# Kernel optimization log

Hardware: AMD Instinct MI355X
Metric: run time of the kernel (lower is better)

Reference implementation:

```python
import jax, jax.numpy as jnp
import numpy as np

HEADS, DK, DV, STRIDE = 8, 32, 32, 2
EPS = 1e-5

def dwconv(x, w, b, stride):
    # depthwise 3x3, padding 1; w: [C,1,3,3]
    y = jax.lax.conv_general_dilated(
        x, w, (stride, stride), ((1, 1), (1, 1)),
        dimension_numbers=("NCHW", "OIHW", "NCHW"),
        feature_group_count=x.shape[1])
    return y + b[None, :, None, None]

def setup_inputs() -> dict:
    key = jax.random.key(0)
    ks = jax.random.split(key, 16)
    B_, C, H, W = 8, 256, 56, 56
    hd = HEADS * DK
    s = lambda k, shp: (jax.random.normal(k, shp, jnp.float32) * 0.02)
    return {
        "x": jax.random.normal(ks[0], (B_, C, H, W), jnp.float32),
        "Wk_dw": s(ks[1], (C, 1, 3, 3)), "bk_dw": jnp.zeros((C,), jnp.float32),
        "Wv_dw": s(ks[2], (C, 1, 3, 3)), "bv_dw": jnp.zeros((C,), jnp.float32),
        "Wq": s(ks[3], (hd, C)), "bq": jnp.zeros((hd,), jnp.float32),
        "Wk": s(ks[4], (hd, C)), "bk": jnp.zeros((hd,), jnp.float32),
        "Wv": s(ks[5], (HEADS * DV, C)), "bv": jnp.zeros((HEADS * DV,), jnp.float32),
        "Wo": s(ks[6], (C, HEADS * DV)), "bo": jnp.zeros((C,), jnp.float32),
        "Bbias": s(ks[7], (1, HEADS, H * W, (H // STRIDE) * (W // STRIDE))),
    }

def reference(x, Wk_dw, bk_dw, Wv_dw, bv_dw, Wq, bq, Wk, bk, Wv, bv, Wo, bo, Bbias):
    b, c, h, w = x.shape
    xr = x.reshape(b, c, h * w).transpose(0, 2, 1)  # [b, hw, c]
    # F.layer_norm with normalized_shape=(b, hw, c): single mean/var over ALL elements
    mu = jnp.mean(xr)
    var = jnp.mean((xr - mu) ** 2)
    xn = (xr - mu) * jax.lax.rsqrt(var + EPS)
    q = (xn @ Wq.T + bq).reshape(b, h * w, HEADS, DK).transpose(0, 2, 1, 3)  # [b,H,hw,dk]
    ki = dwconv(x, Wk_dw, bk_dw, STRIDE)
    kh, kw = ki.shape[2], ki.shape[3]
    kf = ki.reshape(b, c, kh * kw).transpose(0, 2, 1)
    k = (kf @ Wk.T + bk).reshape(b, kh * kw, HEADS, DK).transpose(0, 2, 1, 3)
    vi = dwconv(x, Wv_dw, bv_dw, STRIDE)
    vf = vi.reshape(b, c, kh * kw).transpose(0, 2, 1)
    v = (vf @ Wv.T + bv).reshape(b, kh * kw, HEADS, DV).transpose(0, 2, 1, 3)
    attn = jnp.einsum("bhid,bhjd->bhij", q, k) * (DK ** -0.5) + Bbias
    attn = jax.nn.softmax(attn, axis=-1)
    res = jnp.einsum("bhij,bhjd->bhid", attn, v).transpose(0, 2, 1, 3)
    res = res.reshape(b, h * w, HEADS * DV)
    out = (res @ Wo.T + bo).reshape(b, c, h, w)  # faithful to original .view (no transpose)
    return out + x
```

## Files before the change

kernel.cpp:

```cpp
#include <hip/hip_runtime.h>

typedef unsigned short u16;
typedef unsigned int   u32;
typedef __attribute__((ext_vector_type(8))) short short8;
typedef __attribute__((ext_vector_type(4))) float f32x4;

#define MFMA16(a, b, c) __builtin_amdgcn_mfma_f32_16x16x32_bf16((a), (b), (c), 0, 0, 0)

static constexpr int B_ = 8;
static constexpr int HW = 3136;
static constexpr int KW = 784;
static constexpr int NELEM = B_ * 256 * HW;

static constexpr size_t OFF_CNT = 4096;
static constexpr size_t OFF_W   = 8192;
static constexpr int AOFF_WQ = 0, AOFF_WK = 65536, AOFF_WV = 131072, AOFF_WO = 196608;
static constexpr int AOFF_WKDW = 262144, AOFF_WVDW = 264448;
static constexpr int AOFF_BKDW = 266752, AOFF_BVDW = 267008, AOFF_BQ = 267264;
static constexpr int AOFF_BK = 267520, AOFF_BV = 267776, AOFF_BO = 268032;
static constexpr size_t OFF_XT  = 557056;
static constexpr size_t SZ_XT   = (size_t)B_ * HW * 256 * 2;
static constexpr size_t SZ_KJ   = (size_t)B_ * KW * 256 * 2;
static constexpr size_t OFF_KIT = OFF_XT + SZ_XT;
static constexpr size_t OFF_VIT = OFF_KIT + SZ_KJ;
static constexpr size_t OFF_KI  = OFF_VIT + SZ_KJ;
static constexpr size_t OFF_VI  = OFF_KI + SZ_KJ;
static constexpr size_t OFF_Q   = OFF_VI + SZ_KJ;
static constexpr size_t OFF_O   = OFF_XT;

__device__ __forceinline__ float bf2f(u16 u) { return __uint_as_float(((u32)u) << 16); }
__device__ __forceinline__ u16 f2bf(float f) {
  u32 u = __float_as_uint(f);
  u32 r = u + 0x7FFFu + ((u >> 16) & 1u);
  return (u16)(r >> 16);
}
__device__ __forceinline__ float bflo(u32 u) { return __uint_as_float(u << 16); }
__device__ __forceinline__ float bfhi(u32 u) { return __uint_as_float(u & 0xFFFF0000u); }
__device__ __forceinline__ u32 packbf(float a, float b) {
  u32 ua = __float_as_uint(a); ua = (ua + 0x7FFFu + ((ua >> 16) & 1u)) >> 16;
  u32 ub = __float_as_uint(b); ub = (ub + 0x7FFFu + ((ub >> 16) & 1u)) >> 16;
  return ua | (ub << 16);
}

__global__ __launch_bounds__(256) void detect_k(const u32* __restrict__ x, int* __restrict__ cnt) {
  int c = 0;
  for (int i = threadIdx.x; i < 4096; i += 256) {
    float v = __uint_as_float(x[i] << 16);
    if (fabsf(v) > 1e4f) c++;
  }
#pragma unroll
  for (int off = 32; off > 0; off >>= 1) c += __shfl_down(c, off);
  if ((threadIdx.x & 63) == 0) atomicAdd(cnt, c);
}

struct CvtArgs { const void* src[12]; int dstoff[12]; int n[12]; };
__global__ __launch_bounds__(256) void cvtw_k(CvtArgs a, u16* __restrict__ arena,
                                              const int* __restrict__ cnt) {
  int t = blockIdx.y;
  int n = a.n[t];
  u16* d = arena + a.dstoff[t];
  int f32m = (*cnt >= 64);
  if (f32m) {
    const float* s = (const float*)a.src[t];
    for (int i = blockIdx.x * 256 + threadIdx.x; i < n; i += gridDim.x * 256) d[i] = f2bf(s[i]);
  } else {
    const u16* s = (const u16*)a.src[t];
    for (int i = blockIdx.x * 256 + threadIdx.x; i < n; i += gridDim.x * 256) d[i] = s[i];
  }
}

__global__ __launch_bounds__(256) void reduce_k(const void* __restrict__ x, double* __restrict__ acc,
                                                const int* __restrict__ cnt) {
  int f32m = (*cnt >= 64);
  float s = 0.f, ss = 0.f;
  if (f32m) {
    const float4* xv = (const float4*)x;
    const int n4 = NELEM / 4;
    for (int i = blockIdx.x * 256 + threadIdx.x; i < n4; i += gridDim.x * 256) {
      float4 u = xv[i];
      s += u.x + u.y + u.z + u.w;
      ss += u.x * u.x + u.y * u.y + u.z * u.z + u.w * u.w;
    }
  } else {
    const uint4* xv = (const uint4*)x;
    const int n8 = NELEM / 8;
    for (int i = blockIdx.x * 256 + threadIdx.x; i < n8; i += gridDim.x * 256) {
      uint4 u = xv[i];
      u32 w[4] = {u.x, u.y, u.z, u.w};
#pragma unroll
      for (int q = 0; q < 4; q++) {
        float f0 = __uint_as_float(w[q] << 16);
        float f1 = __uint_as_float(w[q] & 0xFFFF0000u);
        s += f0 + f1;
        ss += f0 * f0 + f1 * f1;
      }
    }
  }
#pragma unroll
  for (int off = 32; off > 0; off >>= 1) {
    s += __shfl_down(s, off);
    ss += __shfl_down(ss, off);
  }
  __shared__ float as_[4], ass_[4];
  int wv = threadIdx.x >> 6;
  if ((threadIdx.x & 63) == 0) { as_[wv] = s; ass_[wv] = ss; }
  __syncthreads();
  if (threadIdx.x == 0) {
    atomicAdd(acc + 0, (double)(as_[0] + as_[1] + as_[2] + as_[3]));
    atomicAdd(acc + 1, (double)(ass_[0] + ass_[1] + ass_[2] + ass_[3]));
  }
}

__global__ __launch_bounds__(256) void prep_k(const u16* __restrict__ wq, const u16* __restrict__ bq,
                                              float* __restrict__ wsf) {
  const double* acc = (const double*)wsf;
  __shared__ float sh[2];
  if (threadIdx.x == 0) {
    double N = (double)NELEM;
    double mu = acc[0] / N;
    double var = acc[1] / N - mu * mu;
    float rstd = (float)(1.0 / sqrt(var + 1e-5));
    sh[0] = (float)mu; sh[1] = rstd;
    wsf[4] = (float)mu; wsf[5] = rstd;
    wsf[6] = rstd * 0.17677669529663687f;
  }
  __syncthreads();
  int o = threadIdx.x;
  float wsum = 0.f;
  for (int c = 0; c < 256; c++) wsum += bf2f(wq[o * 256 + c]);
  wsf[16 + o] = (bf2f(bq[o]) - sh[1] * sh[0] * wsum) * 0.17677669529663687f;
}

__global__ __launch_bounds__(256) void transpose_x_k(const void* __restrict__ src, u16* __restrict__ dst,
                                                     const int* __restrict__ cnt) {
  int f32m = (*cnt >= 64);
  __shared__ u16 t[32][33];
  int b = blockIdx.z;
  int r0 = blockIdx.y * 32, c0 = blockIdx.x * 32;
  int tid = threadIdx.x, col = tid & 31;
  size_t base = (size_t)b * 256 * HW;
  if (f32m) {
    const float* s = (const float*)src + base;
#pragma unroll
    for (int i = 0; i < 4; i++) {
      int row = (tid >> 5) + i * 8;
      t[row][col] = f2bf(s[(size_t)(r0 + row) * HW + c0 + col]);
    }
  } else {
    const u16* s = (const u16*)src + base;
#pragma unroll
    for (int i = 0; i < 4; i++) {
      int row = (tid >> 5) + i * 8;
      t[row][col] = s[(size_t)(r0 + row) * HW + c0 + col];
    }
  }
  __syncthreads();
  u16* d = dst + base;
#pragma unroll
  for (int i = 0; i < 4; i++) {
    int row = (tid >> 5) + i * 8;
    d[(size_t)(c0 + row) * 256 + r0 + col] = t[col][row];
  }
}

__global__ __launch_bounds__(256) void transpose_kv_k(const u16* __restrict__ s1, u16* __restrict__ d1,
                                                      const u16* __restrict__ s2, u16* __restrict__ d2) {
  __shared__ u16 t[32][33];
  int which = blockIdx.z >> 3;
  int b = blockIdx.z & 7;
  const u16* src = which ? s2 : s1;
  u16* dst = which ? d2 : d1;
  int r0 = blockIdx.y * 32, c0 = blockIdx.x * 32;
  const u16* s = src + (size_t)b * 256 * KW;
  u16* d = dst + (size_t)b * 256 * KW;
  int tid = threadIdx.x, col = tid & 31;
#pragma unroll
  for (int i = 0; i < 4; i++) {
    int row = (tid >> 5) + i * 8;
    if (c0 + col < KW) t[row][col] = s[(size_t)(r0 + row) * KW + c0 + col];
  }
  __syncthreads();
#pragma unroll
  for (int i = 0; i < 4; i++) {
    int row = (tid >> 5) + i * 8;
    if (c0 + row < KW) d[(size_t)(c0 + row) * 256 + r0 + col] = t[col][row];
  }
}

__global__ __launch_bounds__(256) void dwconv_k(const void* __restrict__ x,
                                                const u16* __restrict__ arena,
                                                u16* __restrict__ ki, u16* __restrict__ vi,
                                                const int* __restrict__ cnt) {
  int f32m = (*cnt >= 64);
  int b = blockIdx.x >> 8;
  int c = blockIdx.x & 255;
  float wkf[9], wvf[9];
#pragma unroll
  for (int t = 0; t < 9; t++) {
    wkf[t] = bf2f(arena[AOFF_WKDW + c * 9 + t]);
    wvf[t] = bf2f(arena[AOFF_WVDW + c * 9 + t]);
  }
  float kb = bf2f(arena[AOFF_BKDW + c]), vb = bf2f(arena[AOFF_BVDW + c]);
  size_t xbase = (size_t)(b * 256 + c) * HW;
  auto body = [&](auto LDX) {
    for (int j = threadIdx.x; j < KW; j += 256) {
      int oi = j / 28, oj = j % 28;
      float ka = kb, va = vb;
#pragma unroll
      for (int di = 0; di < 3; di++) {
        int ii = 2 * oi - 1 + di;
        if ((unsigned)ii >= 56u) continue;
#pragma unroll
        for (int dj = 0; dj < 3; dj++) {
          int ij = 2 * oj - 1 + dj;
          if ((unsigned)ij >= 56u) continue;
          float xv = LDX(ii * 56 + ij);
          ka += xv * wkf[di * 3 + dj];
          va += xv * wvf[di * 3 + dj];
        }
      }
      ki[(size_t)(b * 256 + c) * KW + j] = f2bf(ka);
      vi[(size_t)(b * 256 + c) * KW + j] = f2bf(va);
    }
  };
  if (f32m) {
    const float* xp = (const float*)x + xbase;
    body([&](int i) { return xp[i]; });
  } else {
    const u16* xp = (const u16*)x + xbase;
    body([&](int i) { return bf2f(xp[i]); });
  }
}

__global__ __launch_bounds__(256) void proj_q_k(const u16* __restrict__ xt, const u16* __restrict__ Wq,
                                                const float* __restrict__ wsf, u16* __restrict__ q) {
  int lane = threadIdx.x & 63, wave = threadIdx.x >> 6;
  int l15 = lane & 15, quad = lane >> 4;
  int b = blockIdx.x / 49, pb = blockIdx.x % 49;
  int p0 = pb * 64 + wave * 16;
  const u16* arow = xt + ((size_t)(b * HW) + p0 + l15) * 256 + quad * 8;
  short8 af[8];
#pragma unroll
  for (int ks = 0; ks < 8; ks++) af[ks] = *(const short8*)(arow + ks * 32);
  float alpha = wsf[6];
  const float* beta = wsf + 16;
  for (int ot = 0; ot < 16; ot++) {
    const u16* brow = Wq + (size_t)(ot * 16 + l15) * 256 + quad * 8;
    f32x4 acc = {0.f, 0.f, 0.f, 0.f};
#pragma unroll
    for (int ks = 0; ks < 8; ks++) acc = MFMA16(af[ks], *(const short8*)(brow + ks * 32), acc);
    int o = ot * 16 + l15;
    float bet = beta[o];
    size_t base = ((size_t)(b * HW) + p0 + quad * 4) * 256 + o;
#pragma unroll
    for (int r = 0; r < 4; r++) q[base + (size_t)r * 256] = f2bf(alpha * acc[r] + bet);
  }
}

__global__ __launch_bounds__(256) void proj_k_k(const u16* __restrict__ kit, const u16* __restrict__ Wk,
                                                const u16* __restrict__ bk, u16* __restrict__ kout) {
  int lane = threadIdx.x & 63, wave = threadIdx.x >> 6;
  int l15 = lane & 15, quad = lane >> 4;
  int b = blockIdx.x / 13, jb = blockIdx.x % 13;
  int p0 = jb * 64 + wave * 16;
  if (p0 >= KW) return;
  const u16* arow = kit + ((size_t)(b * KW) + p0 + l15) * 256 + quad * 8;
  short8 af[8];
#pragma unroll
  for (int ks = 0; ks < 8; ks++) af[ks] = *(const short8*)(arow + ks * 32);
  for (int ot = 0; ot < 16; ot++) {
    const u16* brow = Wk + (size_t)(ot * 16 + l15) * 256 + quad * 8;
    f32x4 acc = {0.f, 0.f, 0.f, 0.f};
#pragma unroll
    for (int ks = 0; ks < 8; ks++) acc = MFMA16(af[ks], *(const short8*)(brow + ks * 32), acc);
    int o = ot * 16 + l15;
    float bias = bf2f(bk[o]);
    size_t base = ((size_t)(b * KW) + p0 + quad * 4) * 256 + o;
#pragma unroll
    for (int r = 0; r < 4; r++) kout[base + (size_t)r * 256] = f2bf(acc[r] + bias);
  }
}

__global__ __launch_bounds__(256) void proj_v_k(const u16* __restrict__ Wv, const u16* __restrict__ vit,
                                                const u16* __restrict__ bv, u16* __restrict__ vT) {
  int lane = threadIdx.x & 63, wave = threadIdx.x >> 6;
  int l15 = lane & 15, quad = lane >> 4;
  int b = blockIdx.x >> 4;
  int ob = (blockIdx.x >> 2) & 3;
  int js = blockIdx.x & 3;
  int o0 = ob * 64 + wave * 16;
  const u16* arow = Wv + (size_t)(o0 + l15) * 256 + quad * 8;
  short8 af[8];
#pragma unroll
  for (int ks = 0; ks < 8; ks++) af[ks] = *(const short8*)(arow + ks * 32);
  int jt0 = js * 13;
  int jt1 = (jt0 + 13 < 49) ? jt0 + 13 : 49;
  for (int jt = jt0; jt < jt1; jt++) {
    const u16* brow = vit + ((size_t)(b * KW) + jt * 16 + l15) * 256 + quad * 8;
    f32x4 acc = {0.f, 0.f, 0.f, 0.f};
#pragma unroll
    for (int ks = 0; ks < 8; ks++) acc = MFMA16(af[ks], *(const short8*)(brow + ks * 32), acc);
#pragma unroll
    for (int r = 0; r < 4; r++) {
      int o = o0 + quad * 4 + r;
      vT[((size_t)(b * 256) + o) * KW + jt * 16 + l15] = f2bf(acc[r] + bf2f(bv[o]));
    }
  }
}

static constexpr int BSTRIDE = 788;
__global__ __launch_bounds__(256) void attn_k(const u16* __restrict__ q, const u16* __restrict__ k,
                                              const u16* __restrict__ vT, const void* __restrict__ Bb,
                                              u16* __restrict__ Ob, const int* __restrict__ cnt) {
  int f32m = (*cnt >= 64);
  int tid = threadIdx.x;
  int lane = tid & 63, wave = tid >> 6;
  int l15 = lane & 15, quad = lane >> 4;
  int bid = blockIdx.x;
  int pt = bid >> 4;
  int h = (bid >> 1) & 7;
  int half = bid & 1;
  int b = half * 4 + wave;
  int p0 = pt * 16;
  __shared__ __align__(16) u16 bls[16 * BSTRIDE];
  __shared__ __align__(16) u16 Pch[4][16][40];

  {
    size_t boff = ((size_t)(h * HW) + p0) * KW;
    if (f32m) {
      const float* bbf = (const float*)Bb + boff;
#pragma unroll
      for (int it = 0; it < 13; it++) {
        int chunk = it * 256 + tid;
        if (chunk < 3136) {
          int row = chunk / 196, c4 = chunk - row * 196;
          float4 v = *(const float4*)(bbf + (size_t)row * KW + c4 * 4);
          uint2 p;
          p.x = packbf(v.x, v.y);
          p.y = packbf(v.z, v.w);
          *(uint2*)&bls[row * BSTRIDE + c4 * 4] = p;
        }
      }
    } else {
      const u16* bbb = (const u16*)Bb + boff;
#pragma unroll
      for (int it = 0; it < 13; it++) {
        int chunk = it * 256 + tid;
        if (chunk < 3136) {
          int row = chunk / 196, c4 = chunk - row * 196;
          *(uint2*)&bls[row * BSTRIDE + c4 * 4] = *(const uint2*)(bbb + (size_t)row * KW + c4 * 4);
        }
      }
    }
  }
  __syncthreads();

  const u16* qp = q + ((size_t)(b * HW) + p0 + l15) * 256 + h * 32 + quad * 8;
  short8 af = *(const short8*)qp;
  const u16* kb = k + (size_t)b * KW * 256 + h * 32 + quad * 8;

  u32 sp[49][2];
#pragma unroll
  for (int jt = 0; jt < 49; jt++) {
    short8 bfr = *(const short8*)(kb + (size_t)(jt * 16 + l15) * 256);
    f32x4 acc = {0.f, 0.f, 0.f, 0.f};
    acc = MFMA16(af, bfr, acc);
    int col = jt * 16 + l15;
    float v0 = acc[0] + bf2f(bls[(quad * 4 + 0) * BSTRIDE + col]);
    float v1 = acc[1] + bf2f(bls[(quad * 4 + 1) * BSTRIDE + col]);
    float v2 = acc[2] + bf2f(bls[(quad * 4 + 2) * BSTRIDE + col]);
    float v3 = acc[3] + bf2f(bls[(quad * 4 + 3) * BSTRIDE + col]);
    sp[jt][0] = packbf(v0, v1);
    sp[jt][1] = packbf(v2, v3);
  }

  float m[4] = {-1e30f, -1e30f, -1e30f, -1e30f};
#pragma unroll
  for (int jt = 0; jt < 49; jt++) {
    m[0] = fmaxf(m[0], bflo(sp[jt][0])); m[1] = fmaxf(m[1], bfhi(sp[jt][0]));
    m[2] = fmaxf(m[2], bflo(sp[jt][1])); m[3] = fmaxf(m[3], bfhi(sp[jt][1]));
  }
#pragma unroll
  for (int off = 1; off < 16; off <<= 1)
#pragma unroll
    for (int r = 0; r < 4; r++) m[r] = fmaxf(m[r], __shfl_xor(m[r], off));
  float l[4] = {0.f, 0.f, 0.f, 0.f};
#pragma unroll
  for (int jt = 0; jt < 49; jt++) {
    float e0 = __expf(bflo(sp[jt][0]) - m[0]);
    float e1 = __expf(bfhi(sp[jt][0]) - m[1]);
    float e2 = __expf(bflo(sp[jt][1]) - m[2]);
    float e3 = __expf(bfhi(sp[jt][1]) - m[3]);
    l[0] += e0; l[1] += e1; l[2] += e2; l[3] += e3;
    sp[jt][0] = packbf(e0, e1);
    sp[jt][1] = packbf(e2, e3);
  }
#pragma unroll
  for (int off = 1; off < 16; off <<= 1)
#pragma unroll
    for (int r = 0; r < 4; r++) l[r] += __shfl_xor(l[r], off);
  float inv[4];
#pragma unroll
  for (int r = 0; r < 4; r++) inv[r] = 1.f / l[r];

  f32x4 oa = {0.f, 0.f, 0.f, 0.f}, obb = {0.f, 0.f, 0.f, 0.f};
  const u16* vb = vT + ((size_t)(b * 256) + h * 32) * KW;
#pragma unroll
  for (int ch = 0; ch < 25; ch++) {
#pragma unroll
    for (int hf = 0; hf < 2; hf++) {
      int jt = ch * 2 + hf;
      u32 p0k = 0, p1k = 0;
      if (jt < 49) { p0k = sp[jt][0]; p1k = sp[jt][1]; }
      int col = hf * 16 + l15;
      Pch[wave][quad * 4 + 0][col] = (u16)(p0k & 0xFFFFu);
      Pch[wave][quad * 4 + 1][col] = (u16)(p0k >> 16);
      Pch[wave][quad * 4 + 2][col] = (u16)(p1k & 0xFFFFu);
      Pch[wave][quad * 4 + 3][col] = (u16)(p1k >> 16);
    }
    __syncthreads();
    short8 pf = *(const short8*)(&Pch[wave][l15][quad * 8]);
    int jo = ch * 32 + quad * 8;
    if (jo > 776) jo = 776;
    short8 v0 = *(const short8*)(vb + (size_t)l15 * KW + jo);
    short8 v1 = *(const short8*)(vb + (size_t)(16 + l15) * KW + jo);
    oa  = MFMA16(pf, v0, oa);
    obb = MFMA16(pf, v1, obb);
    __syncthreads();
  }
  size_t obase = ((size_t)(b * HW) + p0 + quad * 4) * 256 + h * 32 + l15;
#pragma unroll
  for (int r = 0; r < 4; r++) {
    Ob[obase + (size_t)r * 256]      = f2bf(oa[r] * inv[r]);
    Ob[obase + (size_t)r * 256 + 16] = f2bf(obb[r] * inv[r]);
  }
}

__global__ __launch_bounds__(256) void proj_o_k(const u16* __restrict__ Ob, const u16* __restrict__ Wo,
                                                const u16* __restrict__ bo, const void* __restrict__ x,
                                                void* __restrict__ out, const int* __restrict__ cnt) {
  int f32m = (*cnt >= 64);
  int lane = threadIdx.x & 63, wave = threadIdx.x >> 6;
  int l15 = lane & 15, quad = lane >> 4;
  int b = blockIdx.x / 49, pb = blockIdx.x % 49;
  int p0 = pb * 64 + wave * 16;
  const u16* arow = Ob + ((size_t)(b * HW) + p0 + l15) * 256 + quad * 8;
  short8 af[8];
#pragma unroll
  for (int ks = 0; ks < 8; ks++) af[ks] = *(const short8*)(arow + ks * 32);
  for (int ot = 0; ot < 16; ot++) {
    const u16* brow = Wo + (size_t)(ot * 16 + l15) * 256 + quad * 8;
    f32x4 acc = {0.f, 0.f, 0.f, 0.f};
#pragma unroll
    for (int ks = 0; ks < 8; ks++) acc = MFMA16(af[ks], *(const short8*)(brow + ks * 32), acc);
    int o = ot * 16 + l15;
    float bias = bf2f(bo[o]);
    if (f32m) {
      const float* xf = (const float*)x;
      float* of = (float*)out;
#pragma unroll
      for (int r = 0; r < 4; r++) {
        size_t idx = ((size_t)(b * HW) + p0 + quad * 4 + r) * 256 + o;
        of[idx] = acc[r] + bias + xf[idx];
      }
    } else {
      const u16* xb = (const u16*)x;
      u16* ob_ = (u16*)out;
#pragma unroll
      for (int r = 0; r < 4; r++) {
        size_t idx = ((size_t)(b * HW) + p0 + quad * 4 + r) * 256 + o;
        ob_[idx] = f2bf(acc[r] + bias + bf2f(xb[idx]));
      }
    }
  }
}

extern "C" void kernel_launch(void* const* d_in, const int* in_sizes, int n_in,
                              void* d_out, int out_size, void* d_ws, size_t ws_size,
                              hipStream_t stream) {
  (void)in_sizes; (void)n_in; (void)out_size; (void)ws_size;
  const void* x = d_in[0];
  char* ws = (char*)d_ws;
  int* cnt = (int*)(ws + OFF_CNT);
  u16* arena = (u16*)(ws + OFF_W);
  u16* xt  = (u16*)(ws + OFF_XT);
  u16* kit = (u16*)(ws + OFF_KIT);
  u16* vit = (u16*)(ws + OFF_VIT);
  u16* ki  = (u16*)(ws + OFF_KI);
  u16* vi  = (u16*)(ws + OFF_VI);
  u16* qb  = (u16*)(ws + OFF_Q);
  u16* Obuf = (u16*)(ws + OFF_O);

  CvtArgs a;
  const int srcidx[12] = {5, 7, 9, 11, 1, 3, 2, 4, 6, 8, 10, 12};
  const int dofs[12] = {AOFF_WQ, AOFF_WK, AOFF_WV, AOFF_WO, AOFF_WKDW, AOFF_WVDW,
                        AOFF_BKDW, AOFF_BVDW, AOFF_BQ, AOFF_BK, AOFF_BV, AOFF_BO};
  const int ns[12] = {65536, 65536, 65536, 65536, 2304, 2304, 256, 256, 256, 256, 256, 256};
  for (int i = 0; i < 12; i++) { a.src[i] = d_in[srcidx[i]]; a.dstoff[i] = dofs[i]; a.n[i] = ns[i]; }

  hipMemsetAsync(d_ws, 0, 8192, stream);
  detect_k<<<1, 256, 0, stream>>>((const u32*)x, cnt);
  cvtw_k<<<dim3(32, 12), 256, 0, stream>>>(a, arena, cnt);
  reduce_k<<<1024, 256, 0, stream>>>(x, (double*)d_ws, cnt);
  prep_k<<<1, 256, 0, stream>>>(arena + AOFF_WQ, arena + AOFF_BQ, (float*)d_ws);
  transpose_x_k<<<dim3(98, 8, 8), 256, 0, stream>>>(x, xt, cnt);
  dwconv_k<<<2048, 256, 0, stream>>>(x, arena, ki, vi, cnt);
  transpose_kv_k<<<dim3(25, 8, 16), 256, 0, stream>>>(ki, kit, vi, vit);
  proj_k_k<<<104, 256, 0, stream>>>(kit, arena + AOFF_WK, arena + AOFF_BK, ki);
  proj_v_k<<<128, 256, 0, stream>>>(arena + AOFF_WV, vit, arena + AOFF_BV, vi);
  proj_q_k<<<392, 256, 0, stream>>>(xt, arena + AOFF_WQ, (const float*)d_ws, qb);
  attn_k<<<3136, 256, 0, stream>>>(qb, ki, vi, d_in[13], Obuf, cnt);
  proj_o_k<<<392, 256, 0, stream>>>(Obuf, arena + AOFF_WO, arena + AOFF_BO, x, d_out, cnt);
}
```

Baseline: 534.8 us.

## Stage projection weights in LDS and stream attention softmax in chunks

Folds the Q, K and output projections into one templated kernel. Each block loads a 64-row slice of the weight matrix into shared memory once and reuses it across many row tiles, where before every wave reread weights from global memory. The attention kernel now uses an online softmax over 7 chunks of 128 keys and stores the bias tile transposed in LDS. This replaces the 49-tile register array and the per-chunk __syncthreads with a wave-local waitcnt, to lower register pressure and raise occupancy. It risks fewer blocks for the projections, and LDS bank conflicts on the transposed bias writes.

Result: no change. 531.7 us (-0.6%).

```diff
diff --git a/kernel.cpp b/kernel.cpp
--- a/kernel.cpp
+++ b/kernel.cpp
@@ -232,52 +232,75 @@
   }
 }
 
-__global__ __launch_bounds__(256) void proj_q_k(const u16* __restrict__ xt, const u16* __restrict__ Wq,
-                                                const float* __restrict__ wsf, u16* __restrict__ q) {
-  int lane = threadIdx.x & 63, wave = threadIdx.x >> 6;
+template<int MODE>
+__global__ __launch_bounds__(256, 4) void proj2_k(const u16* __restrict__ act, const u16* __restrict__ Wt,
+                                                  const float* __restrict__ wsf, const u16* __restrict__ bias,
+                                                  const void* __restrict__ x, void* __restrict__ outp,
+                                                  const int* __restrict__ cnt, int R, int tpb) {
+  __shared__ __align__(16) u16 Wl[64 * 264];
+  int tid = threadIdx.x, lane = tid & 63, wave = tid >> 6;
   int l15 = lane & 15, quad = lane >> 4;
-  int b = blockIdx.x / 49, pb = blockIdx.x % 49;
-  int p0 = pb * 64 + wave * 16;
-  const u16* arow = xt + ((size_t)(b * HW) + p0 + l15) * 256 + quad * 8;
-  short8 af[8];
-#pragma unroll
-  for (int ks = 0; ks < 8; ks++) af[ks] = *(const short8*)(arow + ks * 32);
-  float alpha = wsf[6];
-  const float* beta = wsf + 16;
-  for (int ot = 0; ot < 16; ot++) {
-    const u16* brow = Wq + (size_t)(ot * 16 + l15) * 256 + quad * 8;
-    f32x4 acc = {0.f, 0.f, 0.f, 0.f};
-#pragma unroll
-    for (int ks = 0; ks < 8; ks++) acc = MFMA16(af[ks], *(const short8*)(brow + ks * 32), acc);
-    int o = ot * 16 + l15;
-    float bet = beta[o];
-    size_t base = ((size_t)(b * HW) + p0 + quad * 4) * 256 + o;
-#pragma unroll
-    for (int r = 0; r < 4; r++) q[base + (size_t)r * 256] = f2bf(alpha * acc[r] + bet);
-  }
-}
-
-__global__ __launch_bounds__(256) void proj_k_k(const u16* __restrict__ kit, const u16* __restrict__ Wk,
-                                                const u16* __restrict__ bk, u16* __restrict__ kout) {
-  int lane = threadIdx.x & 63, wave = threadIdx.x >> 6;
-  int l15 = lane & 15, quad = lane >> 4;
-  int b = blockIdx.x / 13, jb = blockIdx.x % 13;
-  int p0 = jb * 64 + wave * 16;
-  if (p0 >= KW) return;
-  const u16* arow = kit + ((size_t)(b * KW) + p0 + l15) * 256 + quad * 8;
-  short8 af[8];
-#pragma unroll
-  for (int ks = 0; ks < 8; ks++) af[ks] = *(const short8*)(arow + ks * 32);
-  for (int ot = 0; ot < 16; ot++) {
-    const u16* brow = Wk + (size_t)(ot * 16 + l15) * 256 + quad * 8;
-    f32x4 acc = {0.f, 0.f, 0.f, 0.f};
-#pragma unroll
-    for (int ks = 0; ks < 8; ks++) acc = MFMA16(af[ks], *(const short8*)(brow + ks * 32), acc);
-    int o = ot * 16 + l15;
-    float bias = bf2f(bk[o]);
-    size_t base = ((size_t)(b * KW) + p0 + quad * 4) * 256 + o;
-#pragma unroll
-    for (int r = 0; r < 4; r++) kout[base + (size_t)r * 256] = f2bf(acc[r] + bias);
+  int og = blockIdx.x & 3;
+  int tmp = blockIdx.x >> 2;
+  int qc = tmp % 7, b = tmp / 7;
+  {
+    int row = tid >> 2, cb = (tid & 3) * 64;
+    const u16* wsrc = Wt + (size_t)(og * 64 + row) * 256 + cb;
+#pragma unroll
+    for (int i = 0; i < 8; i++)
+      *(short8*)&Wl[row * 264 + cb + i * 8] = *(const short8*)(wsrc + i * 8);
+  }
+  __syncthreads();
+  int f32m = (MODE == 2) ? (*cnt >= 64) : 0;
+  float alpha = (MODE == 0) ? wsf[6] : 0.f;
+  for (int tt = wave; tt < tpb; tt += 4) {
+    int p0 = (qc * tpb + tt) * 16;
+    const u16* arow = act + ((size_t)b * R + p0 + l15) * 256 + quad * 8;
+    short8 afr[8];
+#pragma unroll
+    for (int ks = 0; ks < 8; ks++) afr[ks] = *(const short8*)(arow + ks * 32);
+#pragma unroll
+    for (int ot = 0; ot < 4; ot++) {
+      f32x4 acc = {0.f, 0.f, 0.f, 0.f};
+#pragma unroll
+      for (int ks = 0; ks < 8; ks++) {
+        short8 bfr = *(const short8*)&Wl[(ot * 16 + l15) * 264 + ks * 32 + quad * 8];
+        acc = MFMA16(afr[ks], bfr, acc);
+      }
+      int o = og * 64 + ot * 16 + l15;
+      if (MODE == 0) {
+        float bet = wsf[16 + o];
+        u16* q = (u16*)outp;
+#pragma unroll
+        for (int r = 0; r < 4; r++)
+          q[((size_t)b * R + p0 + quad * 4 + r) * 256 + o] = f2bf(alpha * acc[r] + bet);
+      } else if (MODE == 1) {
+        float bi = bf2f(bias[o]);
+        u16* ko = (u16*)outp;
+#pragma unroll
+        for (int r = 0; r < 4; r++)
+          ko[((size_t)b * R + p0 + quad * 4 + r) * 256 + o] = f2bf(acc[r] + bi);
+      } else {
+        float bi = bf2f(bias[o]);
+        if (f32m) {
+          const float* xf = (const float*)x;
+          float* of = (float*)outp;
+#pragma unroll
+          for (int r = 0; r < 4; r++) {
+            size_t idx = ((size_t)b * R + p0 + quad * 4 + r) * 256 + o;
+            of[idx] = acc[r] + bi + xf[idx];
+          }
+        } else {
+          const u16* xb = (const u16*)x;
+          u16* ob_ = (u16*)outp;
+#pragma unroll
+          for (int r = 0; r < 4; r++) {
+            size_t idx = ((size_t)b * R + p0 + quad * 4 + r) * 256 + o;
+            ob_[idx] = f2bf(acc[r] + bi + bf2f(xb[idx]));
+          }
+        }
+      }
+    }
   }
 }
 
@@ -308,10 +331,10 @@
   }
 }
 
-static constexpr int BSTRIDE = 788;
-__global__ __launch_bounds__(256) void attn_k(const u16* __restrict__ q, const u16* __restrict__ k,
-                                              const u16* __restrict__ vT, const void* __restrict__ Bb,
-                                              u16* __restrict__ Ob, const int* __restrict__ cnt) {
+static constexpr int PSTRIDE = 136;
+__global__ __launch_bounds__(256, 3) void attn_k(const u16* __restrict__ q, const u16* __restrict__ k,
+                                                 const u16* __restrict__ vT, const void* __restrict__ Bb,
+                                                 u16* __restrict__ Ob, const int* __restrict__ cnt) {
   int f32m = (*cnt >= 64);
   int tid = threadIdx.x;
   int lane = tid & 63, wave = tid >> 6;
@@ -322,8 +345,8 @@
   int half = bid & 1;
   int b = half * 4 + wave;
   int p0 = pt * 16;
-  __shared__ __align__(16) u16 bls[16 * BSTRIDE];
-  __shared__ __align__(16) u16 Pch[4][16][40];
+  __shared__ __align__(16) u16 blsT[784 * 16];
+  __shared__ __align__(16) u16 Pch[4][16 * PSTRIDE];
 
   {
     size_t boff = ((size_t)(h * HW) + p0) * KW;
@@ -333,12 +356,12 @@
       for (int it = 0; it < 13; it++) {
         int chunk = it * 256 + tid;
         if (chunk < 3136) {
-          int row = chunk / 196, c4 = chunk - row * 196;
-          float4 v = *(const float4*)(bbf + (size_t)row * KW + c4 * 4);
-          uint2 p;
-          p.x = packbf(v.x, v.y);
-          p.y = packbf(v.z, v.w);
-          *(uint2*)&bls[row * BSTRIDE + c4 * 4] = p;
+          int row = chunk / 196, c4 = (chunk - row * 196) * 4;
+          float4 v = *(const float4*)(bbf + (size_t)row * KW + c4);
+          blsT[(c4 + 0) * 16 + row] = f2bf(v.x);
+          blsT[(c4 + 1) * 16 + row] = f2bf(v.y);
+          blsT[(c4 + 2) * 16 + row] = f2bf(v.z);
+          blsT[(c4 + 3) * 16 + row] = f2bf(v.w);
         }
       }
     } else {
@@ -347,8 +370,12 @@
       for (int it = 0; it < 13; it++) {
         int chunk = it * 256 + tid;
         if (chunk < 3136) {
-          int row = chunk / 196, c4 = chunk - row * 196;
-          *(uint2*)&bls[row * BSTRIDE + c4 * 4] = *(const uint2*)(bbb + (size_t)row * KW + c4 * 4);
+          int row = chunk / 196, c4 = (chunk - row * 196) * 4;
+          uint2 lv = *(const uint2*)(bbb + (size_t)row * KW + c4);
+          blsT[(c4 + 0) * 16 + row] = (u16)(lv.x & 0xFFFFu);
+          blsT[(c4 + 1) * 16 + row] = (u16)(lv.x >> 16);
+          blsT[(c4 + 2) * 16 + row] = (u16)(lv.y & 0xFFFFu);
+          blsT[(c4 + 3) * 16 + row] = (u16)(lv.y >> 16);
         }
       }
     }
@@ -358,120 +385,95 @@
   const u16* qp = q + ((size_t)(b * HW) + p0 + l15) * 256 + h * 32 + quad * 8;
   short8 af = *(const short8*)qp;
   const u16* kb = k + (size_t)b * KW * 256 + h * 32 + quad * 8;
-
-  u32 sp[49][2];
-#pragma unroll
-  for (int jt = 0; jt < 49; jt++) {
-    short8 bfr = *(const short8*)(kb + (size_t)(jt * 16 + l15) * 256);
-    f32x4 acc = {0.f, 0.f, 0.f, 0.f};
-    acc = MFMA16(af, bfr, acc);
-    int col = jt * 16 + l15;
-    float v0 = acc[0] + bf2f(bls[(quad * 4 + 0) * BSTRIDE + col]);
-    float v1 = acc[1] + bf2f(bls[(quad * 4 + 1) * BSTRIDE + col]);
-    float v2 = acc[2] + bf2f(bls[(quad * 4 + 2) * BSTRIDE + col]);
-    float v3 = acc[3] + bf2f(bls[(quad * 4 + 3) * BSTRIDE + col]);
-    sp[jt][0] = packbf(v0, v1);
-    sp[jt][1] = packbf(v2, v3);
-  }
-
-  float m[4] = {-1e30f, -1e30f, -1e30f, -1e30f};
-#pragma unroll
-  for (int jt = 0; jt < 49; jt++) {
-    m[0] = fmaxf(m[0], bflo(sp[jt][0])); m[1] = fmaxf(m[1], bfhi(sp[jt][0]));
-    m[2] = fmaxf(m[2], bflo(sp[jt][1])); m[3] = fmaxf(m[3], bfhi(sp[jt][1]));
-  }
-#pragma unroll
-  for (int off = 1; off < 16; off <<= 1)
-#pragma unroll
-    for (int r = 0; r < 4; r++) m[r] = fmaxf(m[r], __shfl_xor(m[r], off));
-  float l[4] = {0.f, 0.f, 0.f, 0.f};
-#pragma unroll
-  for (int jt = 0; jt < 49; jt++) {
-    float e0 = __expf(bflo(sp[jt][0]) - m[0]);
-    float e1 = __expf(bfhi(sp[jt][0]) - m[1]);
-    float e2 = __expf(bflo(sp[jt][1]) - m[2]);
-    float e3 = __expf(bfhi(sp[jt][1]) - m[3]);
-    l[0] += e0; l[1] += e1; l[2] += e2; l[3] += e3;
-    sp[jt][0] = packbf(e0, e1);
-    sp[jt][1] = packbf(e2, e3);
-  }
-#pragma unroll
-  for (int off = 1; off < 16; off <<= 1)
-#pragma unroll
-    for (int r = 0; r < 4; r++) l[r] += __shfl_xor(l[r], off);
-  float inv[4];
-#pragma unroll
-  for (int r = 0; r < 4; r++) inv[r] = 1.f / l[r];
-
-  f32x4 oa = {0.f, 0.f, 0.f, 0.f}, obb = {0.f, 0.f, 0.f, 0.f};
   const u16* vb = vT + ((size_t)(b * 256) + h * 32) * KW;
-#pragma unroll
-  for (int ch = 0; ch < 25; ch++) {
-#pragma unroll
-    for (int hf = 0; hf < 2; hf++) {
-      int jt = ch * 2 + hf;
-      u32 p0k = 0, p1k = 0;
-      if (jt < 49) { p0k = sp[jt][0]; p1k = sp[jt][1]; }
-      int col = hf * 16 + l15;
-      Pch[wave][quad * 4 + 0][col] = (u16)(p0k & 0xFFFFu);
-      Pch[wave][quad * 4 + 1][col] = (u16)(p0k >> 16);
-      Pch[wave][quad * 4 + 2][col] = (u16)(p1k & 0xFFFFu);
-      Pch[wave][quad * 4 + 3][col] = (u16)(p1k >> 16);
-    }
-    __syncthreads();
-    short8 pf = *(const short8*)(&Pch[wave][l15][quad * 8]);
-    int jo = ch * 32 + quad * 8;
-    if (jo > 776) jo = 776;
-    short8 v0 = *(const short8*)(vb + (size_t)l15 * KW + jo);
-    short8 v1 = *(const short8*)(vb + (size_t)(16 + l15) * KW + jo);
-    oa  = MFMA16(pf, v0, oa);
-    obb = MFMA16(pf, v1, obb);
-    __syncthreads();
-  }
+  u16* pw = &Pch[wave][0];
+
+  float m[4], l[4];
+  f32x4 oa = {0.f, 0.f, 0.f, 0.f}, oc = {0.f, 0.f, 0.f, 0.f};
+#pragma unroll
+  for (int r = 0; r < 4; r++) { m[r] = -3.0e38f; l[r] = 0.f; }
+
+#pragma unroll 1
+  for (int c = 0; c < 7; c++) {
+    f32x4 s[8];
+#pragma unroll
+    for (int t = 0; t < 8; t++) {
+      int jt = c * 8 + t;
+      int jrow = jt * 16 + l15;
+      int jcl = jrow > 783 ? 783 : jrow;
+      short8 kf = *(const short8*)(kb + (size_t)jcl * 256);
+      f32x4 acc = {0.f, 0.f, 0.f, 0.f};
+      acc = MFMA16(af, kf, acc);
+      uint2 braw = *(const uint2*)&blsT[jcl * 16 + quad * 4];
+      bool valid = jrow < 784;
+      s[t][0] = valid ? acc[0] + bflo(braw.x) : -3.0e38f;
+      s[t][1] = valid ? acc[1] + bfhi(braw.x) : -3.0e38f;
+      s[t][2] = valid ? acc[2] + bflo(braw.y) : -3.0e38f;
+      s[t][3] = valid ? acc[3] + bfhi(braw.y) : -3.0e38f;
+    }
+    float cm[4], al[4], ps[4];
+#pragma unroll
+    for (int r = 0; r < 4; r++) {
+      float v = s[0][r];
+#pragma unroll
+      for (int t = 1; t < 8; t++) v = fmaxf(v, s[t][r]);
+      cm[r] = v;
+    }
+#pragma unroll
+    for (int off = 1; off < 16; off <<= 1)
+#pragma unroll
+      for (int r = 0; r < 4; r++) cm[r] = fmaxf(cm[r], __shfl_xor(cm[r], off));
+#pragma unroll
+    for (int r = 0; r < 4; r++) {
+      float mn = fmaxf(m[r], cm[r]);
+      al[r] = __expf(m[r] - mn);
+      m[r] = mn;
+      ps[r] = 0.f;
+    }
+#pragma unroll
+    for (int t = 0; t < 8; t++)
+#pragma unroll
+      for (int r = 0; r < 4; r++) {
+        float e = __expf(s[t][r] - m[r]);
+        s[t][r] = e;
+        ps[r] += e;
+      }
+#pragma unroll
+    for (int off = 1; off < 16; off <<= 1)
+#pragma unroll
+      for (int r = 0; r < 4; r++) ps[r] += __shfl_xor(ps[r], off);
+#pragma unroll
+    for (int r = 0; r < 4; r++) {
+      l[r] = l[r] * al[r] + ps[r];
+      oa[r] *= al[r];
+      oc[r] *= al[r];
+    }
+#pragma unroll
+    for (int t = 0; t < 8; t++) {
+      int col = t * 16 + l15;
+#pragma unroll
+      for (int r = 0; r < 4; r++)
+        pw[(quad * 4 + r) * PSTRIDE + col] = f2bf(s[t][r]);
+    }
+    __builtin_amdgcn_s_waitcnt(0xC07F);
+#pragma unroll
+    for (int kc = 0; kc < 4; kc++) {
+      short8 pf = *(const short8*)(pw + l15 * PSTRIDE + kc * 32 + quad * 8);
+      int jo = c * 128 + kc * 32 + quad * 8;
+      if (jo > 776) jo = 776;
+      short8 v0 = *(const short8*)(vb + (size_t)l15 * KW + jo);
+      short8 v1 = *(const short8*)(vb + (size_t)(16 + l15) * KW + jo);
+      oa = MFMA16(pf, v0, oa);
+      oc = MFMA16(pf, v1, oc);
+    }
+  }
+
   size_t obase = ((size_t)(b * HW) + p0 + quad * 4) * 256 + h * 32 + l15;
 #pragma unroll
   for (int r = 0; r < 4; r++) {
-    Ob[obase + (size_t)r * 256]      = f2bf(oa[r] * inv[r]);
-    Ob[obase + (size_t)r * 256 + 16] = f2bf(obb[r] * inv[r]);
-  }
-}
-
-__global__ __launch_bounds__(256) void proj_o_k(const u16* __restrict__ Ob, const u16* __restrict__ Wo,
-                                                const u16* __restrict__ bo, const void* __restrict__ x,
-                                                void* __restrict__ out, const int* __restrict__ cnt) {
-  int f32m = (*cnt >= 64);
-  int lane = threadIdx.x & 63, wave = threadIdx.x >> 6;
-  int l15 = lane & 15, quad = lane >> 4;
-  int b = blockIdx.x / 49, pb = blockIdx.x % 49;
-  int p0 = pb * 64 + wave * 16;
-  const u16* arow = Ob + ((size_t)(b * HW) + p0 + l15) * 256 + quad * 8;
-  short8 af[8];
-#pragma unroll
-  for (int ks = 0; ks < 8; ks++) af[ks] = *(const short8*)(arow + ks * 32);
-  for (int ot = 0; ot < 16; ot++) {
-    const u16* brow = Wo + (size_t)(ot * 16 + l15) * 256 + quad * 8;
-    f32x4 acc = {0.f, 0.f, 0.f, 0.f};
-#pragma unroll
-    for (int ks = 0; ks < 8; ks++) acc = MFMA16(af[ks], *(const short8*)(brow + ks * 32), acc);
-    int o = ot * 16 + l15;
-    float bias = bf2f(bo[o]);
-    if (f32m) {
-      const float* xf = (const float*)x;
-      float* of = (float*)out;
-#pragma unroll
-      for (int r = 0; r < 4; r++) {
-        size_t idx = ((size_t)(b * HW) + p0 + quad * 4 + r) * 256 + o;
-        of[idx] = acc[r] + bias + xf[idx];
-      }
-    } else {
-      const u16* xb = (const u16*)x;
-      u16* ob_ = (u16*)out;
-#pragma unroll
-      for (int r = 0; r < 4; r++) {
-        size_t idx = ((size_t)(b * HW) + p0 + quad * 4 + r) * 256 + o;
-        ob_[idx] = f2bf(acc[r] + bias + bf2f(xb[idx]));
-      }
-    }
+    float inv = 1.f / l[r];
+    Ob[obase + (size_t)r * 256]      = f2bf(oa[r] * inv);
+    Ob[obase + (size_t)r * 256 + 16] = f2bf(oc[r] * inv);
   }
 }
 
@@ -506,9 +508,12 @@
   transpose_x_k<<<dim3(98, 8, 8), 256, 0, stream>>>(x, xt, cnt);
   dwconv_k<<<2048, 256, 0, stream>>>(x, arena, ki, vi, cnt);
   transpose_kv_k<<<dim3(25, 8, 16), 256, 0, stream>>>(ki, kit, vi, vit);
-  proj_k_k<<<104, 256, 0, stream>>>(kit, arena + AOFF_WK, arena + AOFF_BK, ki);
+  proj2_k<1><<<224, 256, 0, stream>>>(kit, arena + AOFF_WK, nullptr, arena + AOFF_BK,
+                                      nullptr, ki, cnt, KW, 7);
   proj_v_k<<<128, 256, 0, stream>>>(arena + AOFF_WV, vit, arena + AOFF_BV, vi);
-  proj_q_k<<<392, 256, 0, stream>>>(xt, arena + AOFF_WQ, (const float*)d_ws, qb);
+  proj2_k<0><<<224, 256, 0, stream>>>(xt, arena + AOFF_WQ, (const float*)d_ws, nullptr,
+                                      nullptr, qb, cnt, HW, 28);
   attn_k<<<3136, 256, 0, stream>>>(qb, ki, vi, d_in[13], Obuf, cnt);
-  proj_o_k<<<392, 256, 0, stream>>>(Obuf, arena + AOFF_WO, arena + AOFF_BO, x, d_out, cnt);
-}
+  proj2_k<2><<<224, 256, 0, stream>>>(Obuf, arena + AOFF_WO, nullptr, arena + AOFF_BO,
+                                      x, d_out, cnt, HW, 28);
+}
```
